# Kernel optimization log

Measured on AMD Instinct MI355X. Metric: run time of the kernel, lower is better.

## Reference

```python
import jax, jax.numpy as jnp
import numpy as np

N_HEAD = 16
N_KV_HEAD = 8
HEAD_DIM = 64
EPS_NORM = 1e-6


def _rms_norm(x):
    # F.rms_norm without learned weight
    return x * jax.lax.rsqrt(jnp.mean(x * x, axis=-1, keepdims=True) + EPS_NORM)


def _apply_rotary_emb(x, cos, sin):
    # x: [B, T, H, D]; cos/sin: [T, 1, D/2] (broadcast over B and H)
    d = x.shape[-1] // 2
    x1, x2 = x[..., :d], x[..., d:]
    return jnp.concatenate([x1 * cos + x2 * sin, -x1 * sin + x2 * cos], axis=-1)


def setup_inputs() -> dict:
    key = jax.random.key(0)
    ks = jax.random.split(key, 8)
    B, T, C = 2, 2048, 1024
    return {
        "x": jax.random.normal(ks[0], (B, T, C), jnp.float32),
        "cos": jax.random.uniform(ks[1], (T, 1, HEAD_DIM // 2), jnp.float32),
        "sin": jax.random.uniform(ks[2], (T, 1, HEAD_DIM // 2), jnp.float32),
        "Wq": jax.random.normal(ks[3], (N_HEAD * HEAD_DIM, C), jnp.float32) * 0.02,
        "Wk": jax.random.normal(ks[4], (N_KV_HEAD * HEAD_DIM, C), jnp.float32) * 0.02,
        "Wv": jax.random.normal(ks[5], (N_KV_HEAD * HEAD_DIM, C), jnp.float32) * 0.02,
        "Wproj": jax.random.normal(ks[6], (C, C), jnp.float32) * 0.02,
        "w_braid": jax.random.normal(ks[7], (HEAD_DIM,), jnp.float32),
    }


def reference(x, cos, sin, Wq, Wk, Wv, Wproj, w_braid):
    B, T, C = x.shape
    q = (x @ Wq.T).reshape(B, T, N_HEAD, HEAD_DIM)
    k = (x @ Wk.T).reshape(B, T, N_KV_HEAD, HEAD_DIM)
    v = (x @ Wv.T).reshape(B, T, N_KV_HEAD, HEAD_DIM)
    q = _rms_norm(_apply_rotary_emb(q, cos, sin))
    k = _rms_norm(_apply_rotary_emb(k, cos, sin))
    # [B, H, T, D]
    q = q.transpose(0, 2, 1, 3)
    k = k.transpose(0, 2, 1, 3)
    v = v.transpose(0, 2, 1, 3)
    rep = N_HEAD // N_KV_HEAD
    k = jnp.repeat(k, rep, axis=1)  # GQA repeat_kv_heads
    v = jnp.repeat(v, rep, axis=1)
    # rank-1 outer-sum score: s_q[i] + s_k[j]
    s_q = jnp.einsum("bhtd,d->bht", q, w_braid)
    s_k = jnp.einsum("bhsd,d->bhs", k, w_braid)
    scores = s_q[..., :, None] + s_k[..., None, :]  # [B, H, T, T]
    causal = jnp.arange(T)[:, None] >= jnp.arange(T)[None, :]
    scores = jnp.where(causal, scores, -jnp.inf)
    attn = jax.nn.sigmoid(scores)  # non-softmax gating
    y = jnp.einsum("bhts,bhsd->bhtd", attn, v)
    y = y / (T ** 0.5 + 1e-6)
    y = y.transpose(0, 2, 1, 3).reshape(B, T, C)
    return y @ Wproj.T
```

## Files before the change

### kernel.cpp

```cpp
#include <hip/hip_runtime.h>

#define BATCH   2
#define T_LEN   2048
#define C_DIM   1024
#define NH      16
#define NKV     8
#define HD      64

typedef unsigned short u16;
typedef __attribute__((ext_vector_type(8))) short short8;
typedef __attribute__((ext_vector_type(4))) float floatx4;

__device__ __forceinline__ u16 f2bf(float f) {
    union { float f; unsigned u; } v; v.f = f;
    unsigned r = v.u + 0x7FFF + ((v.u >> 16) & 1);
    return (u16)(r >> 16);
}

__device__ __forceinline__ void gload_lds16(const u16* g, u16* l) {
    __builtin_amdgcn_global_load_lds(
        (const __attribute__((address_space(1))) void*)g,
        (__attribute__((address_space(3))) void*)l, 16, 0, 0);
}

__global__ __launch_bounds__(256)
void cvt_all(const float* __restrict__ x, const float* __restrict__ Wq,
             const float* __restrict__ Wk, const float* __restrict__ Wv,
             const float* __restrict__ Wp, u16* __restrict__ xb,
             u16* __restrict__ Wqkvb, u16* __restrict__ Wpb) {
    const int blk = blockIdx.x;
    const float* src; u16* dst; long off;
    if (blk < 4096)      { src = x;  dst = xb;              off = (long)blk * 1024; }
    else if (blk < 5120) { src = Wq; dst = Wqkvb;           off = (long)(blk - 4096) * 1024; }
    else if (blk < 5632) { src = Wk; dst = Wqkvb + 1048576; off = (long)(blk - 5120) * 1024; }
    else if (blk < 6144) { src = Wv; dst = Wqkvb + 1572864; off = (long)(blk - 5632) * 1024; }
    else                 { src = Wp; dst = Wpb;             off = (long)(blk - 6144) * 1024; }
    const long i = off + (long)threadIdx.x * 4;
    const float4 f = *(const float4*)&src[i];
    ushort4 o;
    o.x = f2bf(f.x); o.y = f2bf(f.y); o.z = f2bf(f.z); o.w = f2bf(f.w);
    *(ushort4*)&dst[i] = o;
}

__global__ __launch_bounds__(256)
void gemm_qkv(const u16* __restrict__ A, const u16* __restrict__ B,
              u16* __restrict__ Vt, float* __restrict__ esq,
              float* __restrict__ esk, const float* __restrict__ cosb,
              const float* __restrict__ sinb, const float* __restrict__ wb) {
    const int K = 1024;
    __shared__ u16 As[128 * 64];
    __shared__ u16 Bs[128 * 64];
    const int tid    = threadIdx.x;
    const int lane   = tid & 63;
    const int wave   = tid >> 6;
    const int row_in = lane & 15;
    const int quad   = lane >> 4;
    const int rw     = (wave & 1) * 64;
    const int cw     = (wave >> 1) * 64;
    const int bi   = blockIdx.x;
    const int xcd  = bi & 7;
    const int bj   = bi >> 3;
    const int row0 = (bj >> 1) * 128;
    const int col0 = (xcd * 2 + (bj & 1)) * 128;

    floatx4 acc[4][4] = {};

    const int n    = row_in;
    const int xa   = n & 7;

    for (int k0 = 0; k0 < K; k0 += 64) {
        #pragma unroll
        for (int c = 0; c < 4; ++c) {
            const int l  = c * 256 + tid;
            const int r  = l >> 3;
            const int kc = (l & 7) ^ (r & 7);
            gload_lds16(A + (size_t)(row0 + r) * K + k0 + kc * 8, &As[(size_t)l * 8]);
            gload_lds16(B + (size_t)(col0 + r) * K + k0 + kc * 8, &Bs[(size_t)l * 8]);
        }
        __syncthreads();
        #pragma unroll
        for (int kk = 0; kk < 2; ++kk) {
            const int co = ((kk * 4 + quad) ^ xa) * 8;
            short8 af[4], bf_[4];
            #pragma unroll
            for (int i = 0; i < 4; ++i)
                af[i] = *(const short8*)&As[(rw + 16 * i + n) * 64 + co];
            #pragma unroll
            for (int j = 0; j < 4; ++j)
                bf_[j] = *(const short8*)&Bs[(cw + 16 * j + n) * 64 + co];
            #pragma unroll
            for (int i = 0; i < 4; ++i)
                #pragma unroll
                for (int j = 0; j < 4; ++j)
                    acc[i][j] = __builtin_amdgcn_mfma_f32_16x16x32_bf16(af[i], bf_[j], acc[i][j], 0, 0, 0);
        }
        __syncthreads();
    }

    const int cw_g = col0 + cw;
    const int rw_g = row0 + rw;
    const int ch   = cw_g >> 6;

    if (ch < 24) {
        const float w0 = wb[n], w1 = wb[16 + n], w2 = wb[32 + n], w3 = wb[48 + n];
        #pragma unroll
        for (int i = 0; i < 4; ++i)
            #pragma unroll
            for (int r = 0; r < 4; ++r) {
                const int grow = rw_g + 16 * i + quad * 4 + r;
                const int t = grow & 2047;
                const int b = grow >> 11;
                const float c0 = cosb[t * 32 + n];
                const float c1 = cosb[t * 32 + 16 + n];
                const float s0 = sinb[t * 32 + n];
                const float s1 = sinb[t * 32 + 16 + n];
                const float x0 = acc[i][0][r], x1 = acc[i][1][r];
                const float x2 = acc[i][2][r], x3 = acc[i][3][r];
                const float r0 = fmaf(x0, c0,  x2 * s0);
                const float r1 = fmaf(x1, c1,  x3 * s1);
                const float r2 = fmaf(x2, c0, -x0 * s0);
                const float r3 = fmaf(x3, c1, -x1 * s1);
                float ss = r0 * r0 + r1 * r1 + r2 * r2 + r3 * r3;
                float dt = r0 * w0 + r1 * w1 + r2 * w2 + r3 * w3;
                #pragma unroll
                for (int m = 1; m < 16; m <<= 1) {
                    ss += __shfl_xor(ss, m, 64);
                    dt += __shfl_xor(dt, m, 64);
                }
                const float val = dt * rsqrtf(ss * (1.0f / 64.0f) + 1e-6f);
                const float e = __expf(-fminf(fmaxf(val, -44.0f), 44.0f));
                if (n == 0) {
                    if (ch < 16) esq[((size_t)b * NH + ch) * T_LEN + t] = e;
                    else         esk[((size_t)b * NKV + ch - 16) * T_LEN + t] = e;
                }
            }
    } else {
        const int vcol = cw_g - 1536;
        const int b    = rw_g >> 11;
        const int tb   = (rw_g & 2047) + quad * 4;
        #pragma unroll
        for (int j = 0; j < 4; ++j) {
            const int dg  = vcol + 16 * j + n;
            const int kvh = dg >> 6;
            const int din = dg & 63;
            u16* dstp = Vt + ((size_t)(b * NKV + kvh) * 64 + din) * T_LEN;
            #pragma unroll
            for (int i = 0; i < 4; ++i) {
                ushort4 o;
                o.x = f2bf(acc[i][j][0]);
                o.y = f2bf(acc[i][j][1]);
                o.z = f2bf(acc[i][j][2]);
                o.w = f2bf(acc[i][j][3]);
                *(ushort4*)&dstp[tb + 16 * i] = o;
            }
        }
    }
}

__global__ __launch_bounds__(512)
void braid_attn(const float* __restrict__ esq, const float* __restrict__ esk,
                const u16* __restrict__ Vt, u16* __restrict__ yb) {
    __shared__ u16 Vd[2][4096];
    __shared__ float eskl[128];
    float* red = (float*)&Vd[0][0];

    const int bi   = blockIdx.x;
    const int g    = (bi & 7) * 2 + ((bi >> 8) & 1);
    const int wnd  = (bi >> 3) & 31;
    const int b    = g >> 3;
    const int kvh  = g & 7;
    const int h    = kvh * 2 + (wnd >> 4);
    const int p    = wnd & 15;
    const int bh   = b * 16 + h;
    const int tid  = threadIdx.x;
    const int lane = tid & 63;
    const int wave = tid >> 6;
    const int sg   = wave >> 2;
    const int w4   = wave & 3;
    const int n    = lane & 15;
    const int quad = lane >> 4;
    const int row  = w4 * 16 + n;

    const float* esq_p = esq + (size_t)bh * T_LEN;
    const float* esk_p = esk + ((size_t)b * NKV + kvh) * T_LEN;
    const u16*   vt_b  = Vt + ((size_t)b * NKV + kvh) * 64 * T_LEN;
    const float  inv   = (float)(1.0 / (45.254833995939045 + 1e-6));

    for (int ph = 0; ph < 2; ++ph) {
        const int t0 = (ph ? p : (31 - p)) * 64;
        const float a = esq_p[t0 + row];
        const int send = t0 + 64;
        floatx4 acc[4] = {};

        for (int s0 = 0; s0 < send; s0 += 128) {
            __syncthreads();
            {
                const int r = tid >> 3, gg = tid & 7;
                const int so = (gg ^ (r & 7)) << 3;
                gload_lds16(vt_b + (size_t)r * T_LEN + s0 + so, &Vd[0][(size_t)tid * 8]);
                if (s0 + 64 < send)
                    gload_lds16(vt_b + (size_t)r * T_LEN + s0 + 64 + so, &Vd[1][(size_t)tid * 8]);
            }
            if (tid < 128 && (tid < 64 || s0 + 64 < send))
                eskl[tid] = esk_p[s0 + tid];
            __syncthreads();

            const int s0g = s0 + sg * 64;
            if (s0g < send) {
                const bool diag = (s0g == t0);
                #pragma unroll
                for (int kk = 0; kk < 2; ++kk) {
                    const float* eb = &eskl[sg * 64 + kk * 32 + quad * 8];
                    const float4 e0 = *(const float4*)eb;
                    const float4 e1 = *(const float4*)(eb + 4);
                    const float ev[8] = {e0.x, e0.y, e0.z, e0.w, e1.x, e1.y, e1.z, e1.w};
                    union { unsigned u[4]; short8 s8; } af;
                    #pragma unroll
                    for (int jj = 0; jj < 4; ++jj) {
                        float r0 = __builtin_amdgcn_rcpf(fmaf(ev[2 * jj],     a, 1.0f));
                        float r1 = __builtin_amdgcn_rcpf(fmaf(ev[2 * jj + 1], a, 1.0f));
                        if (diag) {
                            const int s_ = kk * 32 + quad * 8 + 2 * jj;
                            if (s_     > row) r0 = 0.0f;
                            if (s_ + 1 > row) r1 = 0.0f;
                        }
                        af.u[jj] = __builtin_amdgcn_perm(__float_as_uint(r1),
                                                         __float_as_uint(r0), 0x07060302u);
                    }
                    #pragma unroll
                    for (int j = 0; j < 4; ++j) {
                        const short8 bfr = *(const short8*)
                            &Vd[sg][(16 * j + n) * 64 + (((kk * 4 + quad) ^ (n & 7)) << 3)];
                        acc[j] = __builtin_amdgcn_mfma_f32_16x16x32_bf16(af.s8, bfr, acc[j], 0, 0, 0);
                    }
                }
            }
        }

        __syncthreads();
        if (sg == 1) {
            #pragma unroll
            for (int j = 0; j < 4; ++j)
                #pragma unroll
                for (int r = 0; r < 4; ++r)
                    red[(j * 4 + r) * 256 + w4 * 64 + lane] = acc[j][r];
        }
        __syncthreads();
        if (sg == 0) {
            #pragma unroll
            for (int j = 0; j < 4; ++j)
                #pragma unroll
                for (int r = 0; r < 4; ++r) {
                    const float o = acc[j][r] + red[(j * 4 + r) * 256 + w4 * 64 + lane];
                    const int t = t0 + w4 * 16 + quad * 4 + r;
                    yb[((size_t)b * T_LEN + t) * C_DIM + h * HD + 16 * j + n] = f2bf(o * inv);
                }
        }
    }
}

__global__ __launch_bounds__(256)
void gemm_proj(const u16* __restrict__ A, const u16* __restrict__ B,
               float* __restrict__ C, int M, int N, int K) {
    __shared__ u16 As[128 * 64];
    __shared__ u16 Bs[64 * 64];
    const int tid    = threadIdx.x;
    const int lane   = tid & 63;
    const int wave   = tid >> 6;
    const int row_in = lane & 15;
    const int quad   = lane >> 4;
    const int rw     = (wave & 1) * 64;
    const int cw     = (wave >> 1) * 32;
    const int bi   = blockIdx.x;
    const int xcd  = bi & 7;
    const int bj   = bi >> 3;
    const int row0 = (bj >> 1) * 128;
    const int col0 = (xcd * 2 + (bj & 1)) * 64;

    floatx4 acc[4][2] = {};

    const int n  = row_in;
    const int xa = n & 7;

    for (int k0 = 0; k0 < K; k0 += 64) {
        #pragma unroll
        for (int c = 0; c < 4; ++c) {
            const int l  = c * 256 + tid;
            const int r  = l >> 3;
            const int kc = (l & 7) ^ (r & 7);
            gload_lds16(A + (size_t)(row0 + r) * K + k0 + kc * 8, &As[(size_t)l * 8]);
        }
        #pragma unroll
        for (int c = 0; c < 2; ++c) {
            const int l  = c * 256 + tid;
            const int r  = l >> 3;
            const int kc = (l & 7) ^ (r & 7);
            gload_lds16(B + (size_t)(col0 + r) * K + k0 + kc * 8, &Bs[(size_t)l * 8]);
        }
        __syncthreads();
        #pragma unroll
        for (int kk = 0; kk < 2; ++kk) {
            const int co = ((kk * 4 + quad) ^ xa) * 8;
            short8 af[4], bf_[2];
            #pragma unroll
            for (int i = 0; i < 4; ++i)
                af[i] = *(const short8*)&As[(rw + 16 * i + n) * 64 + co];
            #pragma unroll
            for (int j = 0; j < 2; ++j)
                bf_[j] = *(const short8*)&Bs[(cw + 16 * j + n) * 64 + co];
            #pragma unroll
            for (int i = 0; i < 4; ++i)
                #pragma unroll
                for (int j = 0; j < 2; ++j)
                    acc[i][j] = __builtin_amdgcn_mfma_f32_16x16x32_bf16(af[i], bf_[j], acc[i][j], 0, 0, 0);
        }
        __syncthreads();
    }

    #pragma unroll
    for (int i = 0; i < 4; ++i)
        #pragma unroll
        for (int j = 0; j < 2; ++j)
            #pragma unroll
            for (int r = 0; r < 4; ++r)
                C[(size_t)(row0 + rw + 16 * i + quad * 4 + r) * N + col0 + cw + 16 * j + row_in]
                    = acc[i][j][r];
}

extern "C" void kernel_launch(void* const* d_in, const int* in_sizes, int n_in,
                              void* d_out, int out_size, void* d_ws, size_t ws_size,
                              hipStream_t stream) {
    const float* x     = (const float*)d_in[0];
    const float* cosb  = (const float*)d_in[1];
    const float* sinb  = (const float*)d_in[2];
    const float* Wq    = (const float*)d_in[3];
    const float* Wk    = (const float*)d_in[4];
    const float* Wv    = (const float*)d_in[5];
    const float* Wproj = (const float*)d_in[6];
    const float* wb    = (const float*)d_in[7];
    float* out = (float*)d_out;

    char* w = (char*)d_ws;
    u16* xb     = (u16*)w;  w += (size_t)4096 * 1024 * 2;
    u16* Wqkvb  = (u16*)w;  w += (size_t)2048 * 1024 * 2;
    u16* Wpb    = (u16*)w;  w += (size_t)1024 * 1024 * 2;
    u16* yb     = (u16*)w;  w += (size_t)4096 * 1024 * 2;
    u16* VtB    = (u16*)w;  w += (size_t)BATCH * NKV * 64 * T_LEN * 2;
    float* esq  = (float*)w; w += (size_t)BATCH * NH * T_LEN * 4;
    float* esk  = (float*)w; w += (size_t)BATCH * NKV * T_LEN * 4;

    dim3 blk(256);
    cvt_all<<<7168, blk, 0, stream>>>(x, Wq, Wk, Wv, Wproj, xb, Wqkvb, Wpb);
    gemm_qkv<<<512, blk, 0, stream>>>(xb, Wqkvb, VtB, esq, esk, cosb, sinb, wb);
    braid_attn<<<512, dim3(512), 0, stream>>>(esq, esk, VtB, yb);
    gemm_proj<<<512, blk, 0, stream>>>(yb, Wpb, out, 4096, 1024, 1024);
}
```

Before: 155.8 us.

## Double-buffer LDS tiles in QKV GEMM, attention and projection kernels

Adds ping-pong LDS buffers to gemm_qkv, braid_attn and gemm_proj. Each kernel now prefetches the next K-tile (or next V/esk chunk) into the alternate buffer before computing on the current one, and drops one barrier per iteration. The aim is to overlap global-to-LDS loads with MFMA work instead of stalling on them. The cost is doubled LDS per block, plus a separate reduction buffer in the attention kernel, which may reduce occupancy.

```diff
diff --git a/kernel.cpp b/kernel.cpp
--- a/kernel.cpp
+++ b/kernel.cpp
@@ -48,8 +48,8 @@
               float* __restrict__ esk, const float* __restrict__ cosb,
               const float* __restrict__ sinb, const float* __restrict__ wb) {
     const int K = 1024;
-    __shared__ u16 As[128 * 64];
-    __shared__ u16 Bs[128 * 64];
+    __shared__ u16 As[2][128 * 64];
+    __shared__ u16 Bs[2][128 * 64];
     const int tid    = threadIdx.x;
     const int lane   = tid & 63;
     const int wave   = tid >> 6;
@@ -68,26 +68,39 @@
     const int n    = row_in;
     const int xa   = n & 7;
 
+    const int sl_r[4]  = { (0*256+tid)>>3, (1*256+tid)>>3, (2*256+tid)>>3, (3*256+tid)>>3 };
+    const int sl_kc[4] = { ((0*256+tid)&7)^(sl_r[0]&7), ((1*256+tid)&7)^(sl_r[1]&7),
+                           ((2*256+tid)&7)^(sl_r[2]&7), ((3*256+tid)&7)^(sl_r[3]&7) };
+
+    #pragma unroll
+    for (int c = 0; c < 4; ++c) {
+        const int l = c * 256 + tid;
+        gload_lds16(A + (size_t)(row0 + sl_r[c]) * K + sl_kc[c] * 8, &As[0][(size_t)l * 8]);
+        gload_lds16(B + (size_t)(col0 + sl_r[c]) * K + sl_kc[c] * 8, &Bs[0][(size_t)l * 8]);
+    }
+    __syncthreads();
+
+    int cur = 0;
     for (int k0 = 0; k0 < K; k0 += 64) {
-        #pragma unroll
-        for (int c = 0; c < 4; ++c) {
-            const int l  = c * 256 + tid;
-            const int r  = l >> 3;
-            const int kc = (l & 7) ^ (r & 7);
-            gload_lds16(A + (size_t)(row0 + r) * K + k0 + kc * 8, &As[(size_t)l * 8]);
-            gload_lds16(B + (size_t)(col0 + r) * K + k0 + kc * 8, &Bs[(size_t)l * 8]);
-        }
-        __syncthreads();
+        if (k0 + 64 < K) {
+            const int kn = k0 + 64;
+            #pragma unroll
+            for (int c = 0; c < 4; ++c) {
+                const int l = c * 256 + tid;
+                gload_lds16(A + (size_t)(row0 + sl_r[c]) * K + kn + sl_kc[c] * 8, &As[cur ^ 1][(size_t)l * 8]);
+                gload_lds16(B + (size_t)(col0 + sl_r[c]) * K + kn + sl_kc[c] * 8, &Bs[cur ^ 1][(size_t)l * 8]);
+            }
+        }
         #pragma unroll
         for (int kk = 0; kk < 2; ++kk) {
             const int co = ((kk * 4 + quad) ^ xa) * 8;
             short8 af[4], bf_[4];
             #pragma unroll
             for (int i = 0; i < 4; ++i)
-                af[i] = *(const short8*)&As[(rw + 16 * i + n) * 64 + co];
+                af[i] = *(const short8*)&As[cur][(rw + 16 * i + n) * 64 + co];
             #pragma unroll
             for (int j = 0; j < 4; ++j)
-                bf_[j] = *(const short8*)&Bs[(cw + 16 * j + n) * 64 + co];
+                bf_[j] = *(const short8*)&Bs[cur][(cw + 16 * j + n) * 64 + co];
             #pragma unroll
             for (int i = 0; i < 4; ++i)
                 #pragma unroll
@@ -95,6 +108,7 @@
                     acc[i][j] = __builtin_amdgcn_mfma_f32_16x16x32_bf16(af[i], bf_[j], acc[i][j], 0, 0, 0);
         }
         __syncthreads();
+        cur ^= 1;
     }
 
     const int cw_g = col0 + cw;
@@ -160,9 +174,9 @@
 __global__ __launch_bounds__(512)
 void braid_attn(const float* __restrict__ esq, const float* __restrict__ esk,
                 const u16* __restrict__ Vt, u16* __restrict__ yb) {
-    __shared__ u16 Vd[2][4096];
-    __shared__ float eskl[128];
-    float* red = (float*)&Vd[0][0];
+    __shared__ u16 Vd[2][2][4096];
+    __shared__ float eskl[2][128];
+    __shared__ float red[4096];
 
     const int bi   = blockIdx.x;
     const int g    = (bi & 7) * 2 + ((bi >> 8) & 1);
@@ -186,31 +200,39 @@
     const u16*   vt_b  = Vt + ((size_t)b * NKV + kvh) * 64 * T_LEN;
     const float  inv   = (float)(1.0 / (45.254833995939045 + 1e-6));
 
+    const int st_r  = tid >> 3;
+    const int st_so = ((tid & 7) ^ (st_r & 7)) << 3;
+
     for (int ph = 0; ph < 2; ++ph) {
         const int t0 = (ph ? p : (31 - p)) * 64;
         const float a = esq_p[t0 + row];
         const int send = t0 + 64;
         floatx4 acc[4] = {};
 
+        gload_lds16(vt_b + (size_t)st_r * T_LEN + st_so, &Vd[0][0][(size_t)tid * 8]);
+        if (64 < send)
+            gload_lds16(vt_b + (size_t)st_r * T_LEN + 64 + st_so, &Vd[0][1][(size_t)tid * 8]);
+        if (tid < 128 && (tid < 64 || 64 < send))
+            eskl[0][tid] = esk_p[tid];
+        __syncthreads();
+
+        int cur = 0;
         for (int s0 = 0; s0 < send; s0 += 128) {
-            __syncthreads();
-            {
-                const int r = tid >> 3, gg = tid & 7;
-                const int so = (gg ^ (r & 7)) << 3;
-                gload_lds16(vt_b + (size_t)r * T_LEN + s0 + so, &Vd[0][(size_t)tid * 8]);
-                if (s0 + 64 < send)
-                    gload_lds16(vt_b + (size_t)r * T_LEN + s0 + 64 + so, &Vd[1][(size_t)tid * 8]);
-            }
-            if (tid < 128 && (tid < 64 || s0 + 64 < send))
-                eskl[tid] = esk_p[s0 + tid];
-            __syncthreads();
+            const int s0n = s0 + 128;
+            if (s0n < send) {
+                gload_lds16(vt_b + (size_t)st_r * T_LEN + s0n + st_so, &Vd[cur ^ 1][0][(size_t)tid * 8]);
+                if (s0n + 64 < send)
+                    gload_lds16(vt_b + (size_t)st_r * T_LEN + s0n + 64 + st_so, &Vd[cur ^ 1][1][(size_t)tid * 8]);
+                if (tid < 128 && (tid < 64 || s0n + 64 < send))
+                    eskl[cur ^ 1][tid] = esk_p[s0n + tid];
+            }
 
             const int s0g = s0 + sg * 64;
             if (s0g < send) {
                 const bool diag = (s0g == t0);
                 #pragma unroll
                 for (int kk = 0; kk < 2; ++kk) {
-                    const float* eb = &eskl[sg * 64 + kk * 32 + quad * 8];
+                    const float* eb = &eskl[cur][sg * 64 + kk * 32 + quad * 8];
                     const float4 e0 = *(const float4*)eb;
                     const float4 e1 = *(const float4*)(eb + 4);
                     const float ev[8] = {e0.x, e0.y, e0.z, e0.w, e1.x, e1.y, e1.z, e1.w};
@@ -230,14 +252,15 @@
                     #pragma unroll
                     for (int j = 0; j < 4; ++j) {
                         const short8 bfr = *(const short8*)
-                            &Vd[sg][(16 * j + n) * 64 + (((kk * 4 + quad) ^ (n & 7)) << 3)];
+                            &Vd[cur][sg][(16 * j + n) * 64 + (((kk * 4 + quad) ^ (n & 7)) << 3)];
                         acc[j] = __builtin_amdgcn_mfma_f32_16x16x32_bf16(af.s8, bfr, acc[j], 0, 0, 0);
                     }
                 }
             }
-        }
-
-        __syncthreads();
+            __syncthreads();
+            cur ^= 1;
+        }
+
         if (sg == 1) {
             #pragma unroll
             for (int j = 0; j < 4; ++j)
@@ -262,8 +285,8 @@
 __global__ __launch_bounds__(256)
 void gemm_proj(const u16* __restrict__ A, const u16* __restrict__ B,
                float* __restrict__ C, int M, int N, int K) {
-    __shared__ u16 As[128 * 64];
-    __shared__ u16 Bs[64 * 64];
+    __shared__ u16 As[2][128 * 64];
+    __shared__ u16 Bs[2][64 * 64];
     const int tid    = threadIdx.x;
     const int lane   = tid & 63;
     const int wave   = tid >> 6;
@@ -282,32 +305,51 @@
     const int n  = row_in;
     const int xa = n & 7;
 
+    #pragma unroll
+    for (int c = 0; c < 4; ++c) {
+        const int l  = c * 256 + tid;
+        const int r  = l >> 3;
+        const int kc = (l & 7) ^ (r & 7);
+        gload_lds16(A + (size_t)(row0 + r) * K + kc * 8, &As[0][(size_t)l * 8]);
+    }
+    #pragma unroll
+    for (int c = 0; c < 2; ++c) {
+        const int l  = c * 256 + tid;
+        const int r  = l >> 3;
+        const int kc = (l & 7) ^ (r & 7);
+        gload_lds16(B + (size_t)(col0 + r) * K + kc * 8, &Bs[0][(size_t)l * 8]);
+    }
+    __syncthreads();
+
+    int cur = 0;
     for (int k0 = 0; k0 < K; k0 += 64) {
-        #pragma unroll
-        for (int c = 0; c < 4; ++c) {
-            const int l  = c * 256 + tid;
-            const int r  = l >> 3;
-            const int kc = (l & 7) ^ (r & 7);
-            gload_lds16(A + (size_t)(row0 + r) * K + k0 + kc * 8, &As[(size_t)l * 8]);
-        }
-        #pragma unroll
-        for (int c = 0; c < 2; ++c) {
-            const int l  = c * 256 + tid;
-            const int r  = l >> 3;
-            const int kc = (l & 7) ^ (r & 7);
-            gload_lds16(B + (size_t)(col0 + r) * K + k0 + kc * 8, &Bs[(size_t)l * 8]);
-        }
-        __syncthreads();
+        if (k0 + 64 < K) {
+            const int kn = k0 + 64;
+            #pragma unroll
+            for (int c = 0; c < 4; ++c) {
+                const int l  = c * 256 + tid;
+                const int r  = l >> 3;
+                const int kc = (l & 7) ^ (r & 7);
+                gload_lds16(A + (size_t)(row0 + r) * K + kn + kc * 8, &As[cur ^ 1][(size_t)l * 8]);
+            }
+            #pragma unroll
+            for (int c = 0; c < 2; ++c) {
+                const int l  = c * 256 + tid;
+                const int r  = l >> 3;
+                const int kc = (l & 7) ^ (r & 7);
+                gload_lds16(B + (size_t)(col0 + r) * K + kn + kc * 8, &Bs[cur ^ 1][(size_t)l * 8]);
+            }
+        }
         #pragma unroll
         for (int kk = 0; kk < 2; ++kk) {
             const int co = ((kk * 4 + quad) ^ xa) * 8;
             short8 af[4], bf_[2];
             #pragma unroll
             for (int i = 0; i < 4; ++i)
-                af[i] = *(const short8*)&As[(rw + 16 * i + n) * 64 + co];
+                af[i] = *(const short8*)&As[cur][(rw + 16 * i + n) * 64 + co];
             #pragma unroll
             for (int j = 0; j < 2; ++j)
-                bf_[j] = *(const short8*)&Bs[(cw + 16 * j + n) * 64 + co];
+                bf_[j] = *(const short8*)&Bs[cur][(cw + 16 * j + n) * 64 + co];
             #pragma unroll
             for (int i = 0; i < 4; ++i)
                 #pragma unroll
@@ -315,6 +357,7 @@
                     acc[i][j] = __builtin_amdgcn_mfma_f32_16x16x32_bf16(af[i], bf_[j], acc[i][j], 0, 0, 0);
         }
         __syncthreads();
+        cur ^= 1;
     }
 
     #pragma unroll
```

Result: no change. 153.6 us (-1.4%).
